# Kernel optimization log

Measured on AMD Instinct MI355X. Metric: run time of the kernel, lower is better.

Reference implementation:

```python
import jax, jax.numpy as jnp
import numpy as np

EPS = 1e-8


def setup_inputs() -> dict:
    key = jax.random.key(0)
    k1, k2, k3 = jax.random.split(key, 3)
    B, N, M, C = 4, 4096, 16384, 256
    xyz = jax.random.normal(k1, (B * N, 3), dtype=jnp.float32)
    new_xyz = jax.random.normal(k2, (B * M, 3), dtype=jnp.float32)
    feat = jax.random.normal(k3, (B * N, C), dtype=jnp.float32)
    offset = jnp.arange(1, B + 1, dtype=jnp.int64) * N      # [4096, 8192, 12288, 16384]
    new_offset = jnp.arange(1, B + 1, dtype=jnp.int64) * M  # [16384, ..., 65536]
    return {"xyz": xyz, "new_xyz": new_xyz, "feat": feat,
            "offset": offset, "new_offset": new_offset, "k": 3}


def _interpolate(xyz_b, new_xyz_b, feat_b, k):
    # xyz_b: [B,N,3], new_xyz_b: [B,M,3], feat_b: [B,N,C]
    # pairwise squared distances via GEMM: [B,M,N]
    q2 = jnp.sum(new_xyz_b * new_xyz_b, axis=-1, keepdims=True)        # [B,M,1]
    s2 = jnp.sum(xyz_b * xyz_b, axis=-1)[:, None, :]                   # [B,1,N]
    cross = jnp.einsum('bmd,bnd->bmn', new_xyz_b, xyz_b)               # [B,M,N]
    d2 = q2 + s2 - 2.0 * cross                                         # [B,M,N]
    neg_d2, idx = jax.lax.top_k(-d2, k)                                # [B,M,k]
    dist = jnp.sqrt(jnp.maximum(-neg_d2, 1e-12))                       # euclidean, like knnquery
    dist_recip = 1.0 / (dist + EPS)
    weight = dist_recip / jnp.sum(dist_recip, axis=-1, keepdims=True)  # [B,M,k]
    gathered = jax.vmap(lambda f, i: f[i])(feat_b, idx)                # [B,M,k,C]
    return jnp.einsum('bmkc,bmk->bmc', gathered, weight)               # [B,M,C]


def reference(xyz, new_xyz, feat, offset, new_offset, k):
    B = offset.shape[0]
    N = xyz.shape[0] // B
    M = new_xyz.shape[0] // B
    C = feat.shape[1]
    # uniform offsets -> reshape into per-cloud batches
    out = _interpolate(xyz.reshape(B, N, 3), new_xyz.reshape(B, M, 3),
                       feat.reshape(B, N, C), k)
    return out.reshape(B * M, C)
```

## Files before the change

### kernel.cpp

```cpp
#include <hip/hip_runtime.h>
#include <float.h>


#define QPL   2
#define QPB   128
#define SPLIT 8
#define KEY_INIT 0x7FEFFFFFFFFFFFFFULL

typedef float v2f __attribute__((ext_vector_type(2)));

__global__ void pack_pts(const float* __restrict__ xyz,
                         float4* __restrict__ pts, int total) {
    int i = blockIdx.x * blockDim.x + threadIdx.x;
    if (i < total) {
        const float sx = xyz[(size_t)i * 3 + 0];
        const float sy = xyz[(size_t)i * 3 + 1];
        const float sz = xyz[(size_t)i * 3 + 2];
        const float s2 = __fadd_rn(__fadd_rn(__fmul_rn(sx, sx), __fmul_rn(sy, sy)),
                                   __fmul_rn(sz, sz));
        pts[i] = make_float4(sx, sy, sz, s2);
    }
}

__device__ __forceinline__ double mk_key(float d2, int j) {
    unsigned long long u =
        ((unsigned long long)(unsigned)__float_as_uint(d2) << 32) | (unsigned)j;
    return __longlong_as_double(u);
}

template <int CHUNK>
__global__ __launch_bounds__(512, 4) void fp_knn_main(
    const float* __restrict__ new_xyz,
    const float4* __restrict__ pts,
    const float4* __restrict__ feat4,
    float4* __restrict__ out4,
    int N, int blocks_per_batch)
{
    __shared__ double s_k[SPLIT][QPB][3];
    __shared__ float  s_w[QPB][3];
    __shared__ int    s_j[QPB][3];

    int g = blockIdx.x;
    if (gridDim.x == 512 && blocks_per_batch == 128) {
        const int xcd = g & 7, slot = g >> 3;
        g = (xcd >> 1) * 128 + (xcd & 1) * 64 + slot;
    }

    const int tid  = threadIdx.x;
    const int lane = tid & 63;
    const int b    = g / blocks_per_batch;
    const int src_base = b * N;
    const int m0 = g * QPB + lane;
    const int m1 = m0 + 64;

    const float q0x = new_xyz[(size_t)m0 * 3 + 0];
    const float q0y = new_xyz[(size_t)m0 * 3 + 1];
    const float q0z = new_xyz[(size_t)m0 * 3 + 2];
    const float q1x = new_xyz[(size_t)m1 * 3 + 0];
    const float q1y = new_xyz[(size_t)m1 * 3 + 1];
    const float q1z = new_xyz[(size_t)m1 * 3 + 2];
    const float q02 = __fadd_rn(__fadd_rn(__fmul_rn(q0x, q0x), __fmul_rn(q0y, q0y)),
                                __fmul_rn(q0z, q0z));
    const float q12 = __fadd_rn(__fadd_rn(__fmul_rn(q1x, q1x), __fmul_rn(q1y, q1y)),
                                __fmul_rn(q1z, q1z));
    const v2f qx2 = {q0x, q1x};
    const v2f qy2 = {q0y, q1y};
    const v2f qz2 = {q0z, q1z};
    const v2f q22 = {q02, q12};

    const int cw    = tid >> 6;
    const int cbase = cw * CHUNK;
    const float4* __restrict__ cp = pts + src_base + cbase;

    double k00 = __longlong_as_double(KEY_INIT);
    double k01 = k00, k02 = k00;
    double k10 = k00, k11 = k00, k12 = k00;

    constexpr int G  = 8;
    constexpr int NG = CHUNK / G;
    float4 buf[2][G];

    #pragma unroll
    for (int t = 0; t < G; ++t) buf[0][t] = cp[t];

    auto process = [&](const float4 p, int cj) {
        #pragma clang fp contract(off)
        const v2f px = {p.x, p.x};
        const v2f py = {p.y, p.y};
        const v2f pz = {p.z, p.z};
        const v2f pw = {p.w, p.w};
        const v2f t0 = qx2 * px;
        const v2f t1 = qy2 * py;
        const v2f t2 = t0 + t1;
        const v2f t3 = qz2 * pz;
        const v2f cr = t2 + t3;
        const v2f qs = q22 + pw;
        const v2f cc = cr + cr;
        const v2f d2 = qs - cc;
        const double ka = mk_key(d2.x, cj);
        const double kb = mk_key(d2.y, cj);
        const double a0 = fmin(ka, k00);
        const double a1 = fmin(fmax(ka, k00), k01);
        const double a2 = fmin(fmax(ka, k01), k02);
        k00 = a0; k01 = a1; k02 = a2;
        const double b0 = fmin(kb, k10);
        const double b1 = fmin(fmax(kb, k10), k11);
        const double b2 = fmin(fmax(kb, k11), k12);
        k10 = b0; k11 = b1; k12 = b2;
    };

    #pragma unroll 2
    for (int gi = 0; gi < NG - 1; ++gi) {
        const float4* nx = cp + (gi + 1) * G;
        #pragma unroll
        for (int t = 0; t < G; ++t) buf[(gi + 1) & 1][t] = nx[t];
        #pragma unroll
        for (int t = 0; t < G; ++t)
            process(buf[gi & 1][t], cbase + gi * G + t);
    }
    #pragma unroll
    for (int t = 0; t < G; ++t)
        process(buf[(NG - 1) & 1][t], cbase + (NG - 1) * G + t);

    s_k[cw][lane][0]      = k00; s_k[cw][lane][1]      = k01; s_k[cw][lane][2]      = k02;
    s_k[cw][lane + 64][0] = k10; s_k[cw][lane + 64][1] = k11; s_k[cw][lane + 64][2] = k12;
    __syncthreads();

    if (tid < QPB) {
        double m0k = __longlong_as_double(KEY_INIT), m1k = m0k, m2k = m0k;
        #pragma unroll
        for (int ss = 0; ss < SPLIT; ++ss) {
            #pragma unroll
            for (int r = 0; r < 3; ++r) {
                const double d = s_k[ss][tid][r];
                const double n0 = fmin(d, m0k);
                const double n1 = fmin(fmax(d, m0k), m1k);
                const double n2 = fmin(fmax(d, m1k), m2k);
                m0k = n0; m1k = n1; m2k = n2;
            }
        }
        unsigned long long u0 = __double_as_longlong(m0k);
        unsigned long long u1 = __double_as_longlong(m1k);
        unsigned long long u2 = __double_as_longlong(m2k);
        const float d0 = __uint_as_float((unsigned)(u0 >> 32));
        const float d1 = __uint_as_float((unsigned)(u1 >> 32));
        const float d2 = __uint_as_float((unsigned)(u2 >> 32));
        const float e0 = sqrtf(fmaxf(d0, 1e-12f));
        const float e1 = sqrtf(fmaxf(d1, 1e-12f));
        const float e2 = sqrtf(fmaxf(d2, 1e-12f));
        const float r0 = 1.0f / (e0 + 1e-8f);
        const float r1 = 1.0f / (e1 + 1e-8f);
        const float r2 = 1.0f / (e2 + 1e-8f);
        const float rs = r0 + r1 + r2;
        s_w[tid][0] = r0 / rs; s_w[tid][1] = r1 / rs; s_w[tid][2] = r2 / rs;
        s_j[tid][0] = (int)(u0 & 0xffffffffu);
        s_j[tid][1] = (int)(u1 & 0xffffffffu);
        s_j[tid][2] = (int)(u2 & 0xffffffffu);
    }
    __syncthreads();

    const int wv    = tid >> 6;
    const int qbase = g * QPB;
    #pragma unroll 4
    for (int t = 0; t < QPB / SPLIT; ++t) {
        const int qq = wv * (QPB / SPLIT) + t;
        const int   a0 = s_j[qq][0], a1 = s_j[qq][1], a2 = s_j[qq][2];
        const float u0 = s_w[qq][0], u1 = s_w[qq][1], u2 = s_w[qq][2];
        const float4 f0 = feat4[(size_t)(src_base + a0) * 64 + lane];
        const float4 f1 = feat4[(size_t)(src_base + a1) * 64 + lane];
        const float4 f2 = feat4[(size_t)(src_base + a2) * 64 + lane];
        float4 o;
        o.x = u0 * f0.x + u1 * f1.x + u2 * f2.x;
        o.y = u0 * f0.y + u1 * f1.y + u2 * f2.y;
        o.z = u0 * f0.z + u1 * f1.z + u2 * f2.z;
        o.w = u0 * f0.w + u1 * f1.w + u2 * f2.w;
        out4[(size_t)(qbase + qq) * 64 + lane] = o;
    }
}

__global__ void fp_knn_generic(
    const float* __restrict__ new_xyz, const float* __restrict__ xyz,
    const float* __restrict__ feat, float* __restrict__ out,
    int N, int M, int Btot)
{
    const int m = blockIdx.x * blockDim.x + threadIdx.x;
    if (m >= Btot * M) return;
    const int b = m / M;
    const int src_base = b * N;
    const float qx = new_xyz[(size_t)m * 3 + 0];
    const float qy = new_xyz[(size_t)m * 3 + 1];
    const float qz = new_xyz[(size_t)m * 3 + 2];
    const float q2 = __fadd_rn(__fadd_rn(__fmul_rn(qx, qx), __fmul_rn(qy, qy)),
                               __fmul_rn(qz, qz));
    double k0 = __longlong_as_double(KEY_INIT), k1 = k0, k2 = k0;
    for (int j = 0; j < N; ++j) {
        const float sx = xyz[(size_t)(src_base + j) * 3 + 0];
        const float sy = xyz[(size_t)(src_base + j) * 3 + 1];
        const float sz = xyz[(size_t)(src_base + j) * 3 + 2];
        const float s2 = __fadd_rn(__fadd_rn(__fmul_rn(sx, sx), __fmul_rn(sy, sy)),
                                   __fmul_rn(sz, sz));
        const float cross = __fadd_rn(
            __fadd_rn(__fmul_rn(qx, sx), __fmul_rn(qy, sy)), __fmul_rn(qz, sz));
        const float d2 = __fadd_rn(q2, s2) - (cross + cross);
        const double key = mk_key(d2, j);
        const double n0 = fmin(key, k0);
        const double n1 = fmin(fmax(key, k0), k1);
        const double n2 = fmin(fmax(key, k1), k2);
        k0 = n0; k1 = n1; k2 = n2;
    }
    unsigned long long u0 = __double_as_longlong(k0);
    unsigned long long u1 = __double_as_longlong(k1);
    unsigned long long u2 = __double_as_longlong(k2);
    const float e0 = sqrtf(fmaxf(__uint_as_float((unsigned)(u0 >> 32)), 1e-12f));
    const float e1 = sqrtf(fmaxf(__uint_as_float((unsigned)(u1 >> 32)), 1e-12f));
    const float e2 = sqrtf(fmaxf(__uint_as_float((unsigned)(u2 >> 32)), 1e-12f));
    const float r0 = 1.0f / (e0 + 1e-8f);
    const float r1 = 1.0f / (e1 + 1e-8f);
    const float r2 = 1.0f / (e2 + 1e-8f);
    const float rs = r0 + r1 + r2;
    const float w0 = r0 / rs, w1 = r1 / rs, w2 = r2 / rs;
    const int a0 = (int)(u0 & 0xffffffffu), a1 = (int)(u1 & 0xffffffffu),
              a2 = (int)(u2 & 0xffffffffu);
    const int C = 256;
    for (int c = 0; c < C; ++c) {
        out[(size_t)m * C + c] =
            w0 * feat[(size_t)(src_base + a0) * C + c] +
            w1 * feat[(size_t)(src_base + a1) * C + c] +
            w2 * feat[(size_t)(src_base + a2) * C + c];
    }
}

extern "C" void kernel_launch(void* const* d_in, const int* in_sizes, int n_in,
                              void* d_out, int out_size, void* d_ws, size_t ws_size,
                              hipStream_t stream) {
    const float* xyz     = (const float*)d_in[0];
    const float* new_xyz = (const float*)d_in[1];
    const float* feat    = (const float*)d_in[2];
    float* out = (float*)d_out;

    const int B = in_sizes[3];
    const int N = in_sizes[0] / (3 * B);
    const int M = in_sizes[1] / (3 * B);

    const size_t need = (size_t)(B * N) * sizeof(float4);
    const bool fast = (N % SPLIT == 0) && (N / SPLIT == 512) &&
                      (M % QPB == 0) && (ws_size >= need);
    if (fast) {
        pack_pts<<<(B * N + 255) / 256, 256, 0, stream>>>(xyz, (float4*)d_ws, B * N);
        const int blocks = (B * M) / QPB;
        fp_knn_main<512><<<blocks, 512, 0, stream>>>(
            new_xyz, (const float4*)d_ws, (const float4*)feat, (float4*)out,
            N, M / QPB);
    } else {
        fp_knn_generic<<<(B * M + 255) / 256, 256, 0, stream>>>(
            new_xyz, xyz, feat, out, N, M, B);
    }
}
```

Measured before the change: 215.3 us.

## Split kNN into float threshold pass, candidate rescan, and separate gather kernel

```diff
diff --git a/kernel.cpp b/kernel.cpp
--- a/kernel.cpp
+++ b/kernel.cpp
@@ -5,6 +5,7 @@
 #define QPL   2
 #define QPB   128
 #define SPLIT 8
+#define CAP   8
 #define KEY_INIT 0x7FEFFFFFFFFFFFFFULL
 
 typedef float v2f __attribute__((ext_vector_type(2)));
@@ -28,17 +29,56 @@
     return __longlong_as_double(u);
 }
 
+__device__ __forceinline__ v2f dist2_pair(const v2f qx2, const v2f qy2,
+                                          const v2f qz2, const v2f q22,
+                                          const float4 p) {
+    #pragma clang fp contract(off)
+    const v2f px = {p.x, p.x};
+    const v2f py = {p.y, p.y};
+    const v2f pz = {p.z, p.z};
+    const v2f pw = {p.w, p.w};
+    const v2f t0 = qx2 * px;
+    const v2f t1 = qy2 * py;
+    const v2f t2 = t0 + t1;
+    const v2f t3 = qz2 * pz;
+    const v2f cr = t2 + t3;
+    const v2f qs = q22 + pw;
+    const v2f cc = cr + cr;
+    const v2f d2 = qs - cc;
+    return d2;
+}
+
+__device__ __forceinline__ float dist2_scalar(float qx, float qy, float qz,
+                                              float q2, const float4 p) {
+    #pragma clang fp contract(off)
+    const float t0 = qx * p.x;
+    const float t1 = qy * p.y;
+    const float t2 = t0 + t1;
+    const float t3 = qz * p.z;
+    const float cr = t2 + t3;
+    const float qs = q2 + p.w;
+    const float cc = cr + cr;
+    const float d2 = qs - cc;
+    return d2;
+}
+
+__device__ __forceinline__ bool lex_less(float d, int j, float D, int J) {
+    return (d < D) || (d == D && j < J);
+}
+
 template <int CHUNK>
-__global__ __launch_bounds__(512, 4) void fp_knn_main(
+__global__ __launch_bounds__(512, 4) void fp_knn_select(
     const float* __restrict__ new_xyz,
     const float4* __restrict__ pts,
-    const float4* __restrict__ feat4,
-    float4* __restrict__ out4,
+    int4*  __restrict__ jb,
+    float4* __restrict__ wb,
     int N, int blocks_per_batch)
 {
-    __shared__ double s_k[SPLIT][QPB][3];
-    __shared__ float  s_w[QPB][3];
-    __shared__ int    s_j[QPB][3];
+    __shared__ float s_v[SPLIT][QPB][3];
+    __shared__ float s_T[QPB];
+    __shared__ int   s_cnt[QPB];
+    __shared__ float s_sd[QPB][CAP];
+    __shared__ int   s_sj[QPB][CAP];
 
     int g = blockIdx.x;
     if (gridDim.x == 512 && blocks_per_batch == 128) {
@@ -72,33 +112,202 @@
     const int cbase = cw * CHUNK;
     const float4* __restrict__ cp = pts + src_base + cbase;
 
+    float va0 = FLT_MAX, va1 = FLT_MAX, va2 = FLT_MAX;
+    float vb0 = FLT_MAX, vb1 = FLT_MAX, vb2 = FLT_MAX;
+    #pragma unroll 8
+    for (int j = 0; j < CHUNK; ++j) {
+        const float4 p = cp[j];
+        const v2f d2 = dist2_pair(qx2, qy2, qz2, q22, p);
+        const float na0 = fminf(d2.x, va0);
+        const float na1 = fminf(fmaxf(d2.x, va0), va1);
+        const float na2 = fminf(fmaxf(d2.x, va1), va2);
+        va0 = na0; va1 = na1; va2 = na2;
+        const float nb0 = fminf(d2.y, vb0);
+        const float nb1 = fminf(fmaxf(d2.y, vb0), vb1);
+        const float nb2 = fminf(fmaxf(d2.y, vb1), vb2);
+        vb0 = nb0; vb1 = nb1; vb2 = nb2;
+    }
+    s_v[cw][lane][0]      = va0; s_v[cw][lane][1]      = va1; s_v[cw][lane][2]      = va2;
+    s_v[cw][lane + 64][0] = vb0; s_v[cw][lane + 64][1] = vb1; s_v[cw][lane + 64][2] = vb2;
+    __syncthreads();
+
+    if (tid < QPB) {
+        float m0v = FLT_MAX, m1v = FLT_MAX, m2v = FLT_MAX;
+        #pragma unroll
+        for (int ss = 0; ss < SPLIT; ++ss) {
+            #pragma unroll
+            for (int r = 0; r < 3; ++r) {
+                const float d = s_v[ss][tid][r];
+                const float n0 = fminf(d, m0v);
+                const float n1 = fminf(fmaxf(d, m0v), m1v);
+                const float n2 = fminf(fmaxf(d, m1v), m2v);
+                m0v = n0; m1v = n1; m2v = n2;
+            }
+        }
+        s_T[tid] = m2v;
+        s_cnt[tid] = 0;
+    }
+    __syncthreads();
+
+    {
+        const float Ta = s_T[lane];
+        const float Tb = s_T[lane + 64];
+        #pragma unroll 8
+        for (int j = 0; j < CHUNK; ++j) {
+            const float4 p = cp[j];
+            const v2f d2 = dist2_pair(qx2, qy2, qz2, q22, p);
+            const bool ha = (d2.x <= Ta);
+            const bool hb = (d2.y <= Tb);
+            if (__any(ha || hb)) {
+                if (ha) {
+                    const int slot = atomicAdd(&s_cnt[lane], 1);
+                    if (slot < CAP) { s_sd[lane][slot] = d2.x; s_sj[lane][slot] = cbase + j; }
+                }
+                if (hb) {
+                    const int slot = atomicAdd(&s_cnt[lane + 64], 1);
+                    if (slot < CAP) { s_sd[lane + 64][slot] = d2.y; s_sj[lane + 64][slot] = cbase + j; }
+                }
+            }
+        }
+    }
+    __syncthreads();
+
+    if (tid < QPB) {
+        const int q = tid;
+        const int cnt = s_cnt[q];
+        float bd0 = FLT_MAX, bd1 = FLT_MAX, bd2 = FLT_MAX;
+        int   bj0 = 0x7fffffff, bj1 = 0x7fffffff, bj2 = 0x7fffffff;
+        if (cnt <= CAP) {
+            for (int i = 0; i < cnt; ++i) {
+                const float d = s_sd[q][i];
+                const int   j = s_sj[q][i];
+                if (lex_less(d, j, bd2, bj2)) {
+                    if (lex_less(d, j, bd1, bj1)) {
+                        bd2 = bd1; bj2 = bj1;
+                        if (lex_less(d, j, bd0, bj0)) {
+                            bd1 = bd0; bj1 = bj0; bd0 = d; bj0 = j;
+                        } else { bd1 = d; bj1 = j; }
+                    } else { bd2 = d; bj2 = j; }
+                }
+            }
+        } else {
+            const int mq = g * QPB + q;
+            const float qx = new_xyz[(size_t)mq * 3 + 0];
+            const float qy = new_xyz[(size_t)mq * 3 + 1];
+            const float qz = new_xyz[(size_t)mq * 3 + 2];
+            const float q2 = __fadd_rn(
+                __fadd_rn(__fmul_rn(qx, qx), __fmul_rn(qy, qy)), __fmul_rn(qz, qz));
+            for (int j = 0; j < N; ++j) {
+                const float4 p = pts[src_base + j];
+                const float d2 = dist2_scalar(qx, qy, qz, q2, p);
+                if (lex_less(d2, j, bd2, bj2)) {
+                    if (lex_less(d2, j, bd1, bj1)) {
+                        bd2 = bd1; bj2 = bj1;
+                        if (lex_less(d2, j, bd0, bj0)) {
+                            bd1 = bd0; bj1 = bj0; bd0 = d2; bj0 = j;
+                        } else { bd1 = d2; bj1 = j; }
+                    } else { bd2 = d2; bj2 = j; }
+                }
+            }
+        }
+        const float e0 = sqrtf(fmaxf(bd0, 1e-12f));
+        const float e1 = sqrtf(fmaxf(bd1, 1e-12f));
+        const float e2 = sqrtf(fmaxf(bd2, 1e-12f));
+        const float r0 = 1.0f / (e0 + 1e-8f);
+        const float r1 = 1.0f / (e1 + 1e-8f);
+        const float r2 = 1.0f / (e2 + 1e-8f);
+        const float rs = r0 + r1 + r2;
+        const int mq = g * QPB + q;
+        jb[mq] = make_int4(bj0, bj1, bj2, 0);
+        wb[mq] = make_float4(r0 / rs, r1 / rs, r2 / rs, 0.0f);
+    }
+}
+
+__global__ __launch_bounds__(256, 8) void fp_gather(
+    const float4* __restrict__ feat4,
+    const int4*  __restrict__ jb,
+    const float4* __restrict__ wb,
+    float4* __restrict__ out4,
+    int N, int M)
+{
+    const int tid  = threadIdx.x;
+    const int lane = tid & 63;
+    const int wv   = tid >> 6;
+    const int qblk = blockIdx.x * 16;
+    const int b    = qblk / M;
+    const int src_base = b * N;
+    #pragma unroll
+    for (int t = 0; t < 4; ++t) {
+        const int q = qblk + wv * 4 + t;
+        const int4   J = jb[q];
+        const float4 W = wb[q];
+        const float4 f0 = feat4[(size_t)(src_base + J.x) * 64 + lane];
+        const float4 f1 = feat4[(size_t)(src_base + J.y) * 64 + lane];
+        const float4 f2 = feat4[(size_t)(src_base + J.z) * 64 + lane];
+        const float u0 = W.x, u1 = W.y, u2 = W.z;
+        float4 o;
+        o.x = u0 * f0.x + u1 * f1.x + u2 * f2.x;
+        o.y = u0 * f0.y + u1 * f1.y + u2 * f2.y;
+        o.z = u0 * f0.z + u1 * f1.z + u2 * f2.z;
+        o.w = u0 * f0.w + u1 * f1.w + u2 * f2.w;
+        out4[(size_t)q * 64 + lane] = o;
+    }
+}
+
+template <int CHUNK>
+__global__ __launch_bounds__(512, 4) void fp_knn_main(
+    const float* __restrict__ new_xyz,
+    const float4* __restrict__ pts,
+    const float4* __restrict__ feat4,
+    float4* __restrict__ out4,
+    int N, int blocks_per_batch)
+{
+    __shared__ double s_k[SPLIT][QPB][3];
+    __shared__ float  s_w[QPB][3];
+    __shared__ int    s_j[QPB][3];
+
+    int g = blockIdx.x;
+    if (gridDim.x == 512 && blocks_per_batch == 128) {
+        const int xcd = g & 7, slot = g >> 3;
+        g = (xcd >> 1) * 128 + (xcd & 1) * 64 + slot;
+    }
+
+    const int tid  = threadIdx.x;
+    const int lane = tid & 63;
+    const int b    = g / blocks_per_batch;
+    const int src_base = b * N;
+    const int m0 = g * QPB + lane;
+    const int m1 = m0 + 64;
+
+    const float q0x = new_xyz[(size_t)m0 * 3 + 0];
+    const float q0y = new_xyz[(size_t)m0 * 3 + 1];
+    const float q0z = new_xyz[(size_t)m0 * 3 + 2];
+    const float q1x = new_xyz[(size_t)m1 * 3 + 0];
+    const float q1y = new_xyz[(size_t)m1 * 3 + 1];
+    const float q1z = new_xyz[(size_t)m1 * 3 + 2];
+    const float q02 = __fadd_rn(__fadd_rn(__fmul_rn(q0x, q0x), __fmul_rn(q0y, q0y)),
+                                __fmul_rn(q0z, q0z));
+    const float q12 = __fadd_rn(__fadd_rn(__fmul_rn(q1x, q1x), __fmul_rn(q1y, q1y)),
+                                __fmul_rn(q1z, q1z));
+    const v2f qx2 = {q0x, q1x};
+    const v2f qy2 = {q0y, q1y};
+    const v2f qz2 = {q0z, q1z};
+    const v2f q22 = {q02, q12};
+
+    const int cw    = tid >> 6;
+    const int cbase = cw * CHUNK;
+    const float4* __restrict__ cp = pts + src_base + cbase;
+
     double k00 = __longlong_as_double(KEY_INIT);
     double k01 = k00, k02 = k00;
     double k10 = k00, k11 = k00, k12 = k00;
 
-    constexpr int G  = 8;
-    constexpr int NG = CHUNK / G;
-    float4 buf[2][G];
-
-    #pragma unroll
-    for (int t = 0; t < G; ++t) buf[0][t] = cp[t];
-
-    auto process = [&](const float4 p, int cj) {
-        #pragma clang fp contract(off)
-        const v2f px = {p.x, p.x};
-        const v2f py = {p.y, p.y};
-        const v2f pz = {p.z, p.z};
-        const v2f pw = {p.w, p.w};
-        const v2f t0 = qx2 * px;
-        const v2f t1 = qy2 * py;
-        const v2f t2 = t0 + t1;
-        const v2f t3 = qz2 * pz;
-        const v2f cr = t2 + t3;
-        const v2f qs = q22 + pw;
-        const v2f cc = cr + cr;
-        const v2f d2 = qs - cc;
-        const double ka = mk_key(d2.x, cj);
-        const double kb = mk_key(d2.y, cj);
+    #pragma unroll 8
+    for (int j = 0; j < CHUNK; ++j) {
+        const float4 p = cp[j];
+        const v2f d2 = dist2_pair(qx2, qy2, qz2, q22, p);
+        const double ka = mk_key(d2.x, cbase + j);
+        const double kb = mk_key(d2.y, cbase + j);
         const double a0 = fmin(ka, k00);
         const double a1 = fmin(fmax(ka, k00), k01);
         const double a2 = fmin(fmax(ka, k01), k02);
@@ -107,20 +316,7 @@
         const double b1 = fmin(fmax(kb, k10), k11);
         const double b2 = fmin(fmax(kb, k11), k12);
         k10 = b0; k11 = b1; k12 = b2;
-    };
-
-    #pragma unroll 2
-    for (int gi = 0; gi < NG - 1; ++gi) {
-        const float4* nx = cp + (gi + 1) * G;
-        #pragma unroll
-        for (int t = 0; t < G; ++t) buf[(gi + 1) & 1][t] = nx[t];
-        #pragma unroll
-        for (int t = 0; t < G; ++t)
-            process(buf[gi & 1][t], cbase + gi * G + t);
-    }
-    #pragma unroll
-    for (int t = 0; t < G; ++t)
-        process(buf[(NG - 1) & 1][t], cbase + (NG - 1) * G + t);
+    }
 
     s_k[cw][lane][0]      = k00; s_k[cw][lane][1]      = k01; s_k[cw][lane][2]      = k02;
     s_k[cw][lane + 64][0] = k10; s_k[cw][lane + 64][1] = k11; s_k[cw][lane + 64][2] = k12;
@@ -199,9 +395,8 @@
         const float sz = xyz[(size_t)(src_base + j) * 3 + 2];
         const float s2 = __fadd_rn(__fadd_rn(__fmul_rn(sx, sx), __fmul_rn(sy, sy)),
                                    __fmul_rn(sz, sz));
-        const float cross = __fadd_rn(
-            __fadd_rn(__fmul_rn(qx, sx), __fmul_rn(qy, sy)), __fmul_rn(qz, sz));
-        const float d2 = __fadd_rn(q2, s2) - (cross + cross);
+        const float4 p = make_float4(sx, sy, sz, s2);
+        const float d2 = dist2_scalar(qx, qy, qz, q2, p);
         const double key = mk_key(d2, j);
         const double n0 = fmin(key, k0);
         const double n1 = fmin(fmax(key, k0), k1);
@@ -242,17 +437,32 @@
     const int N = in_sizes[0] / (3 * B);
     const int M = in_sizes[1] / (3 * B);
 
-    const size_t need = (size_t)(B * N) * sizeof(float4);
-    const bool fast = (N % SPLIT == 0) && (N / SPLIT == 512) &&
-                      (M % QPB == 0) && (ws_size >= need);
-    if (fast) {
+    const int Q = B * M;
+    const size_t pts_bytes = (size_t)(B * N) * sizeof(float4);
+    const size_t jb_bytes  = (size_t)Q * sizeof(int4);
+    const size_t wb_bytes  = (size_t)Q * sizeof(float4);
+    const size_t need_split = pts_bytes + jb_bytes + wb_bytes;
+
+    const bool shape_ok = (N % SPLIT == 0) && (N / SPLIT == 512) &&
+                          (M % QPB == 0) && (M % 16 == 0);
+    if (shape_ok && ws_size >= need_split) {
+        float4* pts = (float4*)d_ws;
+        int4*   jb  = (int4*)((char*)d_ws + pts_bytes);
+        float4* wb  = (float4*)((char*)d_ws + pts_bytes + jb_bytes);
+        pack_pts<<<(B * N + 255) / 256, 256, 0, stream>>>(xyz, pts, B * N);
+        const int blocks = Q / QPB;
+        fp_knn_select<512><<<blocks, 512, 0, stream>>>(
+            new_xyz, pts, jb, wb, N, M / QPB);
+        fp_gather<<<Q / 16, 256, 0, stream>>>(
+            (const float4*)feat, jb, wb, (float4*)out, N, M);
+    } else if (shape_ok && ws_size >= pts_bytes) {
         pack_pts<<<(B * N + 255) / 256, 256, 0, stream>>>(xyz, (float4*)d_ws, B * N);
-        const int blocks = (B * M) / QPB;
+        const int blocks = Q / QPB;
         fp_knn_main<512><<<blocks, 512, 0, stream>>>(
             new_xyz, (const float4*)d_ws, (const float4*)feat, (float4*)out,
             N, M / QPB);
     } else {
-        fp_knn_generic<<<(B * M + 255) / 256, 256, 0, stream>>>(
+        fp_knn_generic<<<(Q + 255) / 256, 256, 0, stream>>>(
             new_xyz, xyz, feat, out, N, M, B);
     }
 }
```

New measurement: 277.0 us. +28.7%, slower.
